# Optimization experiments

Measured on AMD Instinct MI355X. Metric: run time of the kernel, lower is better.

## Reference

```python
import jax, jax.numpy as jnp
import numpy as np
from jax import lax

N, D, K = 8192, 512, 16
EPS = 1e-8


def _safe_sqrt(x):
    # sqrt with a guard so vjp is finite at exact zeros (diagonal of dist matrix)
    return jnp.where(x > 0, jnp.sqrt(jnp.maximum(x, 1e-12)), 0.0)


def _pairwise_dist(a):
    # [n, d] -> [n, n] euclidean distances via Gram trick
    sq = jnp.sum(a * a, axis=-1)
    d2 = sq[:, None] + sq[None, :] - 2.0 * (a @ a.T)
    return _safe_sqrt(d2)


def _curvature_proxy(emb, k):
    n = emb.shape[0]
    dists = _pairwise_dist(emb)  # [n, n]
    neg_d, knn_idx = lax.top_k(-dists, k + 1)  # k+1 smallest
    knn_dists = -neg_d[:, 1:]   # drop self [n, k]
    knn_idx = knn_idx[:, 1:]    # [n, k]
    avg_dist_to_neighbors = knn_dists.mean(axis=1)  # [n]

    nb = emb[knn_idx]  # [n, k, d] gathered neighbor embeddings
    nsq = jnp.sum(nb * nb, axis=-1)  # [n, k]
    gram = jnp.einsum('nkd,nld->nkl', nb, nb)  # [n, k, k]
    inter = _safe_sqrt(nsq[:, :, None] + nsq[:, None, :] - 2.0 * gram)

    mask = jnp.triu(jnp.ones((k, k), dtype=bool), 1)
    n_pairs = k * (k - 1) // 2
    inter_mean = jnp.sum(jnp.where(mask, inter, 0.0), axis=(1, 2)) / n_pairs  # [n]

    curvature = inter_mean / (avg_dist_to_neighbors + EPS)
    return curvature, knn_dists


def setup_inputs() -> dict:
    key = jax.random.key(0)
    k1, k2, k3 = jax.random.split(key, 3)
    embeddings = jax.random.normal(k1, (N, D), dtype=jnp.float32)
    ref_curvature = jax.random.uniform(k2, (N,), dtype=jnp.float32)
    ref_distances = jax.random.uniform(k3, (N, K), dtype=jnp.float32)
    return {"embeddings": embeddings, "ref_curvature": ref_curvature,
            "ref_distances": ref_distances}


def reference(embeddings, ref_curvature, ref_distances):
    curr_curv, curr_dists = _curvature_proxy(embeddings, K)
    curvature_loss = jnp.mean((curr_curv - ref_curvature) ** 2)
    scale_loss = (curr_dists.mean() - ref_distances.mean()) ** 2
    return curvature_loss + 0.1 * scale_loss
```

## Files before the change

kernel.cpp:

```cpp
#include <hip/hip_runtime.h>
#include <cfloat>
#include <cmath>
#include <stdint.h>

#define N 8192
#define D 512
#define K 16
#define RB 128
#define JS 2048
#define NSL (N / JS)
#define JT 128
#define KC 64
#define NCH (D / KC)
#define CAP 32
#define PB 64

typedef __bf16 bf16x8 __attribute__((ext_vector_type(8)));
typedef __bf16 bf16x4 __attribute__((ext_vector_type(4)));
typedef float  f32x16 __attribute__((ext_vector_type(16)));
typedef float  f32x4  __attribute__((ext_vector_type(4)));

__global__ __launch_bounds__(256)
void k_cast_sqnorm(const float* __restrict__ emb, float* __restrict__ sq,
                   __bf16* __restrict__ embh) {
    int row = blockIdx.x * 4 + (threadIdx.x >> 6);
    int lane = threadIdx.x & 63;
    const float4* e = (const float4*)(emb + (size_t)row * D);
    float s = 0.f;
    #pragma unroll
    for (int c = 0; c < 2; c++) {
        float4 v = e[lane + 64 * c];
        s += v.x * v.x + v.y * v.y + v.z * v.z + v.w * v.w;
        bf16x4 h = { (__bf16)v.x, (__bf16)v.y, (__bf16)v.z, (__bf16)v.w };
        *(bf16x4*)&embh[(size_t)row * D + (size_t)(lane + 64 * c) * 4] = h;
    }
    for (int off = 32; off; off >>= 1) s += __shfl_down(s, off, 64);
    if (lane == 0) sq[row] = s;
}

__global__ __launch_bounds__(512)
void k_knn(const __bf16* __restrict__ embh, const float* __restrict__ sq,
           float* __restrict__ pd2, int* __restrict__ pidx) {
    __shared__ __align__(16) __bf16 As[2][RB][KC + 8];
    __shared__ __align__(16) __bf16 Bs[2][JT][KC + 8];
    __shared__ float svD[RB][CAP + 1];
    __shared__ int   svI[RB][CAP + 1];
    __shared__ float sqr[RB];
    __shared__ float kadj[RB];
    __shared__ int   scount[RB];
    __shared__ int   again;

    const int t   = threadIdx.x;
    const int rg  = blockIdx.x >> 2;
    const int sl  = blockIdx.x & 3;
    const int ib  = rg * RB;
    const int jsb = sl * JS;
    const int lane = t & 63, quad = lane >> 5, l31 = lane & 31;
    const int w  = t >> 6;
    const int wr = (w & 3) * 32;
    const int wc = (w >> 2) * 64;

    const int mrow = t >> 2, tid4 = t & 3;
    float l0 = FLT_MAX, l1 = FLT_MAX, l2 = FLT_MAX, l3 = FLT_MAX;
    int   i0 = 0, i1 = 0, i2 = 0, i3 = 0;
    float kmx = FLT_MAX;

    if (t < RB) {
        sqr[t] = sq[ib + t];
        kadj[t] = FLT_MAX; scount[t] = 0;
    }
    __syncthreads();

    for (int jt = 0; jt < JS / JT; jt++) {
        const int jb = jsb + jt * JT;
        f32x16 zero = {};
        f32x16 acc[2];
        acc[0] = zero; acc[1] = zero;

        #pragma unroll
        for (int q = 0; q < 2; q++) {
            int s = t + 512 * q;
            int row = s >> 3, g = s & 7;
            *(uint4*)&As[0][row][g * 8] = *(const uint4*)&embh[(size_t)(ib + row) * D + g * 8];
            *(uint4*)&Bs[0][row][g * 8] = *(const uint4*)&embh[(size_t)(jb + row) * D + g * 8];
        }
        __syncthreads();

        uint4 pfA[2], pfB[2];
        for (int kc = 0; kc < NCH; kc++) {
            const int cur = kc & 1;
            if (kc + 1 < NCH) {
                int k0 = (kc + 1) * KC;
                #pragma unroll
                for (int q = 0; q < 2; q++) {
                    int s = t + 512 * q; int row = s >> 3, g = s & 7;
                    pfA[q] = *(const uint4*)&embh[(size_t)(ib + row) * D + k0 + g * 8];
                    pfB[q] = *(const uint4*)&embh[(size_t)(jb + row) * D + k0 + g * 8];
                }
            }
            #pragma unroll
            for (int kk = 0; kk < KC / 16; kk++) {
                int ko = kk * 16 + quad * 8;
                bf16x8 a0 = *(const bf16x8*)&As[cur][wr + l31][ko];
                bf16x8 b0 = *(const bf16x8*)&Bs[cur][wc + l31][ko];
                bf16x8 b1 = *(const bf16x8*)&Bs[cur][wc + 32 + l31][ko];
                acc[0] = __builtin_amdgcn_mfma_f32_32x32x16_bf16(a0, b0, acc[0], 0, 0, 0);
                acc[1] = __builtin_amdgcn_mfma_f32_32x32x16_bf16(a0, b1, acc[1], 0, 0, 0);
            }
            if (kc + 1 < NCH) {
                #pragma unroll
                for (int q = 0; q < 2; q++) {
                    int s = t + 512 * q; int row = s >> 3, g = s & 7;
                    *(uint4*)&As[cur ^ 1][row][g * 8] = pfA[q];
                    *(uint4*)&Bs[cur ^ 1][row][g * 8] = pfB[q];
                }
            }
            __syncthreads();
        }

        float sqc0 = sq[jb + wc + l31];
        float sqc1 = sq[jb + wc + 32 + l31];
        uint32_t mask = 0;
        while (true) {
            if (t == 0) again = 0;
            #pragma unroll
            for (int c = 0; c < 2; c++)
            #pragma unroll
            for (int reg = 0; reg < 16; reg++) {
                int bit = (c << 4) | reg;
                if ((mask >> bit) & 1) continue;
                int row_l = wr + ((reg & 3) + ((reg >> 2) << 3) + (quad << 2));
                float t2 = (c ? sqc1 : sqc0) - 2.f * acc[c][reg];
                if (t2 < kadj[row_l]) {
                    int j = jb + wc + c * 32 + l31;
                    if (j != ib + row_l) {
                        int p = atomicAdd(&scount[row_l], 1);
                        if (p < CAP) {
                            svD[row_l][p] = t2 + sqr[row_l];
                            svI[row_l][p] = j;
                            mask |= (1u << bit);
                        }
                    }
                }
            }
            __syncthreads();
            {
                int cnt = scount[mrow];
                if (cnt) {
                    int m = cnt < CAP ? cnt : CAP;
                    for (int p = 0; p < m; p++) {
                        float d2 = svD[mrow][p];
                        if (d2 < kmx) {
                            float mx = l0; int am = 0;
                            if (l1 > mx) { mx = l1; am = 1; }
                            if (l2 > mx) { mx = l2; am = 2; }
                            if (l3 > mx) { mx = l3; am = 3; }
                            int gam = (tid4 << 2) | am;
                            float omx = __shfl_xor(mx, 1, 64);
                            int   oga = __shfl_xor(gam, 1, 64);
                            if (omx > mx || (omx == mx && oga < gam)) { mx = omx; gam = oga; }
                            omx = __shfl_xor(mx, 2, 64);
                            oga = __shfl_xor(gam, 2, 64);
                            if (omx > mx || (omx == mx && oga < gam)) { mx = omx; gam = oga; }
                            if ((gam >> 2) == tid4) {
                                int jv = svI[mrow][p];
                                int ls = gam & 3;
                                if      (ls == 0) { l0 = d2; i0 = jv; }
                                else if (ls == 1) { l1 = d2; i1 = jv; }
                                else if (ls == 2) { l2 = d2; i2 = jv; }
                                else              { l3 = d2; i3 = jv; }
                            }
                            float lm = fmaxf(fmaxf(l0, l1), fmaxf(l2, l3));
                            lm = fmaxf(lm, __shfl_xor(lm, 1, 64));
                            lm = fmaxf(lm, __shfl_xor(lm, 2, 64));
                            kmx = lm;
                        }
                    }
                    if (tid4 == 0) {
                        kadj[mrow] = kmx - sqr[mrow];
                        scount[mrow] = 0;
                        if (cnt > CAP) again = 1;
                    }
                }
            }
            __syncthreads();
            int more = again;
            __syncthreads();
            if (!more) break;
        }
    }

    {
        size_t base = (size_t)(ib + mrow) * (NSL * K) + sl * K + tid4 * 4;
        pd2[base + 0] = l0; pd2[base + 1] = l1; pd2[base + 2] = l2; pd2[base + 3] = l3;
        pidx[base + 0] = i0; pidx[base + 1] = i1; pidx[base + 2] = i2; pidx[base + 3] = i3;
    }
}

__global__ __launch_bounds__(256)
void k_merge(const float* __restrict__ pd2, const int* __restrict__ pidx,
             int* __restrict__ knn, float* __restrict__ row_sum) {
    int row = blockIdx.x * 256 + threadIdx.x;
    float bd[K]; int bi[K];
    #pragma unroll
    for (int q = 0; q < K; q++) { bd[q] = FLT_MAX; bi[q] = 0; }
    float kmx = FLT_MAX;
    const float* pr = pd2 + (size_t)row * (NSL * K);
    const int*   pi = pidx + (size_t)row * (NSL * K);
    for (int s = 0; s < NSL * K; s++) {
        float d2 = pr[s];
        if (d2 < kmx) {
            int am = 0; float mx = bd[0];
            #pragma unroll
            for (int q = 1; q < K; q++) if (bd[q] > mx) { mx = bd[q]; am = q; }
            bd[am] = d2; bi[am] = pi[s];
            mx = bd[0];
            #pragma unroll
            for (int q = 1; q < K; q++) mx = fmaxf(mx, bd[q]);
            kmx = mx;
        }
    }
    float s = 0.f;
    #pragma unroll
    for (int q = 0; q < K; q++) {
        float d2 = bd[q];
        s += (d2 > 0.f) ? sqrtf(fmaxf(d2, 1e-12f)) : 0.f;
        knn[(size_t)row * K + q] = bi[q];
    }
    row_sum[row] = s;
}

__global__ __launch_bounds__(256)
void k_curv(const __bf16* __restrict__ embh, const int* __restrict__ knn_idx,
            const float* __restrict__ row_sum, const float* __restrict__ ref_curv,
            float* __restrict__ curv_err) {
    __shared__ float diagS[4][16];
    const int t = threadIdx.x;
    const int w = t >> 6, lane = t & 63;
    const int i = blockIdx.x * 4 + w;

    const int nidx = knn_idx[(size_t)i * K + (lane & 15)];
    const __bf16* src = embh + (size_t)nidx * D + (lane >> 4) * 8;

    f32x4 acc = {};
    #pragma unroll
    for (int kc = 0; kc < D / 32; kc++) {
        bf16x8 a = *(const bf16x8*)(src + kc * 32);
        acc = __builtin_amdgcn_mfma_f32_16x16x32_bf16(a, a, acc, 0, 0, 0);
    }

    #pragma unroll
    for (int q = 0; q < 4; q++) {
        int r = (lane >> 4) * 4 + q;
        if (r == (lane & 15)) diagS[w][r] = acc[q];
    }
    __syncthreads();

    float s = 0.f;
    #pragma unroll
    for (int q = 0; q < 4; q++) {
        int r = (lane >> 4) * 4 + q, c = lane & 15;
        if (r != c) {
            float d2 = diagS[w][r] + diagS[w][c] - 2.f * acc[q];
            s += (d2 > 0.f) ? sqrtf(fmaxf(d2, 1e-12f)) : 0.f;
        }
    }
    #pragma unroll
    for (int off = 32; off; off >>= 1) s += __shfl_down(s, off, 64);

    if (lane == 0) {
        float inter_mean = (0.5f * s) / 120.f;
        float avg = row_sum[i] / 16.f;
        float curv = inter_mean / (avg + 1e-8f);
        float diff = curv - ref_curv[i];
        curv_err[i] = diff * diff;
    }
}

__global__ __launch_bounds__(256)
void k_part(const float* __restrict__ curv_err, const float* __restrict__ row_sum,
            const float* __restrict__ ref_dist, float* __restrict__ part) {
    const int b = blockIdx.x, t = threadIdx.x;
    const int gid = b * 256 + t;
    const int stride = PB * 256;
    float s1 = 0.f, s2 = 0.f, s3 = 0.f;
    for (int i = gid; i < N; i += stride) { s1 += curv_err[i]; s2 += row_sum[i]; }
    for (int i = gid; i < N * K; i += stride) s3 += ref_dist[i];
    for (int off = 32; off; off >>= 1) {
        s1 += __shfl_down(s1, off, 64);
        s2 += __shfl_down(s2, off, 64);
        s3 += __shfl_down(s3, off, 64);
    }
    __shared__ float a1[4], a2[4], a3[4];
    int w = t >> 6, lane = t & 63;
    if (lane == 0) { a1[w] = s1; a2[w] = s2; a3[w] = s3; }
    __syncthreads();
    if (t == 0) {
        float t1 = 0.f, t2 = 0.f, t3 = 0.f;
        #pragma unroll
        for (int q = 0; q < 4; q++) { t1 += a1[q]; t2 += a2[q]; t3 += a3[q]; }
        part[b] = t1; part[PB + b] = t2; part[2 * PB + b] = t3;
    }
}

__global__ __launch_bounds__(64)
void k_final2(const float* __restrict__ part, float* __restrict__ out) {
    const int t = threadIdx.x;
    float s1 = part[t], s2 = part[PB + t], s3 = part[2 * PB + t];
    for (int off = 32; off; off >>= 1) {
        s1 += __shfl_down(s1, off, 64);
        s2 += __shfl_down(s2, off, 64);
        s3 += __shfl_down(s3, off, 64);
    }
    if (t == 0) {
        float curv_loss = s1 / (float)N;
        float dm = s2 / (float)(N * K);
        float rm = s3 / (float)(N * K);
        float d = dm - rm;
        out[0] = curv_loss + 0.1f * d * d;
    }
}

extern "C" void kernel_launch(void* const* d_in, const int* in_sizes, int n_in,
                              void* d_out, int out_size, void* d_ws, size_t ws_size,
                              hipStream_t stream) {
    const float* emb      = (const float*)d_in[0];
    const float* ref_curv = (const float*)d_in[1];
    const float* ref_dist = (const float*)d_in[2];
    float* out = (float*)d_out;

    float*  sq       = (float*)d_ws;
    float*  row_sum  = sq + N;
    float*  curv_err = row_sum + N;
    float*  pd2      = curv_err + N;
    int*    pidx     = (int*)(pd2 + (size_t)N * NSL * K);
    int*    knn      = pidx + (size_t)N * NSL * K;
    __bf16* embh     = (__bf16*)(knn + (size_t)N * K);
    float*  part     = (float*)(embh + (size_t)N * D);

    k_cast_sqnorm<<<N / 4, 256, 0, stream>>>(emb, sq, embh);
    k_knn<<<(N / RB) * NSL, 512, 0, stream>>>(embh, sq, pd2, pidx);
    k_merge<<<N / 256, 256, 0, stream>>>(pd2, pidx, knn, row_sum);
    k_curv<<<N / 4, 256, 0, stream>>>(embh, knn, row_sum, ref_curv, curv_err);
    k_part<<<PB, 256, 0, stream>>>(curv_err, row_sum, ref_dist, part);
    k_final2<<<1, 64, 0, stream>>>(part, out);
}
```

Before: 422.6 us.

## Halve KNN row block to 64 rows with 8 threads per row top-k

```diff
diff --git a/kernel.cpp b/kernel.cpp
--- a/kernel.cpp
+++ b/kernel.cpp
@@ -6,7 +6,7 @@
 #define N 8192
 #define D 512
 #define K 16
-#define RB 128
+#define RB 64
 #define JS 2048
 #define NSL (N / JS)
 #define JT 128
@@ -57,12 +57,12 @@
     const int jsb = sl * JS;
     const int lane = t & 63, quad = lane >> 5, l31 = lane & 31;
     const int w  = t >> 6;
-    const int wr = (w & 3) * 32;
-    const int wc = (w >> 2) * 64;
-
-    const int mrow = t >> 2, tid4 = t & 3;
-    float l0 = FLT_MAX, l1 = FLT_MAX, l2 = FLT_MAX, l3 = FLT_MAX;
-    int   i0 = 0, i1 = 0, i2 = 0, i3 = 0;
+    const int wr = (w & 1) * 32;
+    const int wc = (w >> 1) * 32;
+
+    const int mrow = t >> 3, tid8 = t & 7;
+    float l0 = FLT_MAX, l1 = FLT_MAX;
+    int   i0 = 0, i1 = 0;
     float kmx = FLT_MAX;
 
     if (t < RB) {
@@ -73,29 +73,33 @@
 
     for (int jt = 0; jt < JS / JT; jt++) {
         const int jb = jsb + jt * JT;
-        f32x16 zero = {};
-        f32x16 acc[2];
-        acc[0] = zero; acc[1] = zero;
-
-        #pragma unroll
-        for (int q = 0; q < 2; q++) {
-            int s = t + 512 * q;
-            int row = s >> 3, g = s & 7;
+        f32x16 acc = {};
+
+        {
+            int row = t >> 3, g = t & 7;
             *(uint4*)&As[0][row][g * 8] = *(const uint4*)&embh[(size_t)(ib + row) * D + g * 8];
-            *(uint4*)&Bs[0][row][g * 8] = *(const uint4*)&embh[(size_t)(jb + row) * D + g * 8];
+            #pragma unroll
+            for (int q = 0; q < 2; q++) {
+                int s = t + 512 * q;
+                int brow = s >> 3, bg = s & 7;
+                *(uint4*)&Bs[0][brow][bg * 8] = *(const uint4*)&embh[(size_t)(jb + brow) * D + bg * 8];
+            }
         }
         __syncthreads();
 
-        uint4 pfA[2], pfB[2];
+        uint4 pfA, pfB[2];
         for (int kc = 0; kc < NCH; kc++) {
             const int cur = kc & 1;
             if (kc + 1 < NCH) {
                 int k0 = (kc + 1) * KC;
+                {
+                    int row = t >> 3, g = t & 7;
+                    pfA = *(const uint4*)&embh[(size_t)(ib + row) * D + k0 + g * 8];
+                }
                 #pragma unroll
                 for (int q = 0; q < 2; q++) {
-                    int s = t + 512 * q; int row = s >> 3, g = s & 7;
-                    pfA[q] = *(const uint4*)&embh[(size_t)(ib + row) * D + k0 + g * 8];
-                    pfB[q] = *(const uint4*)&embh[(size_t)(jb + row) * D + k0 + g * 8];
+                    int s = t + 512 * q; int brow = s >> 3, bg = s & 7;
+                    pfB[q] = *(const uint4*)&embh[(size_t)(jb + brow) * D + k0 + bg * 8];
                 }
             }
             #pragma unroll
@@ -103,42 +107,39 @@
                 int ko = kk * 16 + quad * 8;
                 bf16x8 a0 = *(const bf16x8*)&As[cur][wr + l31][ko];
                 bf16x8 b0 = *(const bf16x8*)&Bs[cur][wc + l31][ko];
-                bf16x8 b1 = *(const bf16x8*)&Bs[cur][wc + 32 + l31][ko];
-                acc[0] = __builtin_amdgcn_mfma_f32_32x32x16_bf16(a0, b0, acc[0], 0, 0, 0);
-                acc[1] = __builtin_amdgcn_mfma_f32_32x32x16_bf16(a0, b1, acc[1], 0, 0, 0);
+                acc = __builtin_amdgcn_mfma_f32_32x32x16_bf16(a0, b0, acc, 0, 0, 0);
             }
             if (kc + 1 < NCH) {
+                {
+                    int row = t >> 3, g = t & 7;
+                    *(uint4*)&As[cur ^ 1][row][g * 8] = pfA;
+                }
                 #pragma unroll
                 for (int q = 0; q < 2; q++) {
-                    int s = t + 512 * q; int row = s >> 3, g = s & 7;
-                    *(uint4*)&As[cur ^ 1][row][g * 8] = pfA[q];
-                    *(uint4*)&Bs[cur ^ 1][row][g * 8] = pfB[q];
+                    int s = t + 512 * q; int brow = s >> 3, bg = s & 7;
+                    *(uint4*)&Bs[cur ^ 1][brow][bg * 8] = pfB[q];
                 }
             }
             __syncthreads();
         }
 
         float sqc0 = sq[jb + wc + l31];
-        float sqc1 = sq[jb + wc + 32 + l31];
         uint32_t mask = 0;
         while (true) {
             if (t == 0) again = 0;
             #pragma unroll
-            for (int c = 0; c < 2; c++)
-            #pragma unroll
             for (int reg = 0; reg < 16; reg++) {
-                int bit = (c << 4) | reg;
-                if ((mask >> bit) & 1) continue;
+                if ((mask >> reg) & 1) continue;
                 int row_l = wr + ((reg & 3) + ((reg >> 2) << 3) + (quad << 2));
-                float t2 = (c ? sqc1 : sqc0) - 2.f * acc[c][reg];
+                float t2 = sqc0 - 2.f * acc[reg];
                 if (t2 < kadj[row_l]) {
-                    int j = jb + wc + c * 32 + l31;
+                    int j = jb + wc + l31;
                     if (j != ib + row_l) {
                         int p = atomicAdd(&scount[row_l], 1);
                         if (p < CAP) {
                             svD[row_l][p] = t2 + sqr[row_l];
                             svI[row_l][p] = j;
-                            mask |= (1u << bit);
+                            mask |= (1u << reg);
                         }
                     }
                 }
@@ -153,30 +154,26 @@
                         if (d2 < kmx) {
                             float mx = l0; int am = 0;
                             if (l1 > mx) { mx = l1; am = 1; }
-                            if (l2 > mx) { mx = l2; am = 2; }
-                            if (l3 > mx) { mx = l3; am = 3; }
-                            int gam = (tid4 << 2) | am;
-                            float omx = __shfl_xor(mx, 1, 64);
-                            int   oga = __shfl_xor(gam, 1, 64);
-                            if (omx > mx || (omx == mx && oga < gam)) { mx = omx; gam = oga; }
-                            omx = __shfl_xor(mx, 2, 64);
-                            oga = __shfl_xor(gam, 2, 64);
-                            if (omx > mx || (omx == mx && oga < gam)) { mx = omx; gam = oga; }
-                            if ((gam >> 2) == tid4) {
+                            int gam = (tid8 << 1) | am;
+                            #pragma unroll
+                            for (int off = 1; off < 8; off <<= 1) {
+                                float omx = __shfl_xor(mx, off, 64);
+                                int   oga = __shfl_xor(gam, off, 64);
+                                if (omx > mx || (omx == mx && oga < gam)) { mx = omx; gam = oga; }
+                            }
+                            if ((gam >> 1) == tid8) {
                                 int jv = svI[mrow][p];
-                                int ls = gam & 3;
-                                if      (ls == 0) { l0 = d2; i0 = jv; }
-                                else if (ls == 1) { l1 = d2; i1 = jv; }
-                                else if (ls == 2) { l2 = d2; i2 = jv; }
-                                else              { l3 = d2; i3 = jv; }
+                                if ((gam & 1) == 0) { l0 = d2; i0 = jv; }
+                                else                { l1 = d2; i1 = jv; }
                             }
-                            float lm = fmaxf(fmaxf(l0, l1), fmaxf(l2, l3));
-                            lm = fmaxf(lm, __shfl_xor(lm, 1, 64));
-                            lm = fmaxf(lm, __shfl_xor(lm, 2, 64));
+                            float lm = fmaxf(l0, l1);
+                            #pragma unroll
+                            for (int off = 1; off < 8; off <<= 1)
+                                lm = fmaxf(lm, __shfl_xor(lm, off, 64));
                             kmx = lm;
                         }
                     }
-                    if (tid4 == 0) {
+                    if (tid8 == 0) {
                         kadj[mrow] = kmx - sqr[mrow];
                         scount[mrow] = 0;
                         if (cnt > CAP) again = 1;
@@ -191,9 +188,9 @@
     }
 
     {
-        size_t base = (size_t)(ib + mrow) * (NSL * K) + sl * K + tid4 * 4;
-        pd2[base + 0] = l0; pd2[base + 1] = l1; pd2[base + 2] = l2; pd2[base + 3] = l3;
-        pidx[base + 0] = i0; pidx[base + 1] = i1; pidx[base + 2] = i2; pidx[base + 3] = i3;
+        size_t base = (size_t)(ib + mrow) * (NSL * K) + sl * K + tid8 * 2;
+        pd2[base + 0] = l0; pd2[base + 1] = l1;
+        pidx[base + 0] = i0; pidx[base + 1] = i1;
     }
 }
 
```

New measurement: 386.0 us. -8.7%, faster.
